# Kernel optimization log

Measured on AMD Instinct MI355X. Metric: run time of the kernel, lower is better.

The kernel has to match this reference:

```python
import jax, jax.numpy as jnp
import numpy as np

N = 100000   # nodes
E = 400000   # edges per relation
K = 2        # n_hop relations
D = 256      # in_dim
ATT = 64     # att_dim
L = 3        # n_layer
H1, H2 = 128, 64
EPS = 1e-5
NEG_SLOPE = 0.01


def setup_inputs() -> dict:
    key = jax.random.key(0)
    ks = jax.random.split(key, 16)
    s = 1.0 / np.sqrt(D)
    return {
        "x": jax.random.normal(ks[0], (N, D), jnp.float32),
        "edges_index": jax.random.randint(ks[1], (K, 2, E), 0, N),
        "edges_weight": jax.random.uniform(ks[2], (K, E), jnp.float32),
        "bn_gamma": jnp.ones((D,), jnp.float32),
        "bn_beta": jnp.zeros((D,), jnp.float32),
        "gcn_W": jax.random.normal(ks[3], (L, D, D), jnp.float32) * s,
        "gcn_b": jnp.zeros((L, D), jnp.float32),
        "att_lin_W": jax.random.normal(ks[4], (L, K, D, ATT), jnp.float32) * s,
        "att_lin_b": jnp.zeros((L, K, ATT), jnp.float32),
        "att_q": jax.random.normal(ks[5], (L, K, ATT), jnp.float32) * (1.0 / np.sqrt(ATT)),
        "proj_W1": jax.random.normal(ks[6], (D, H1), jnp.float32) * s,
        "proj_b1": jnp.zeros((H1,), jnp.float32),
        "proj_W2": jax.random.normal(ks[7], (H1, H2), jnp.float32) * (1.0 / np.sqrt(H1)),
        "proj_b2": jnp.zeros((H2,), jnp.float32),
    }


def _gcn_aggregate(row, col, w, xw):
    # symmetric gcn_norm on adj_t (add_self_loops=False):
    # deg[i] = sum of w over edges with col == i
    deg = jax.ops.segment_sum(w, col, num_segments=N)
    dinv = jnp.where(deg > 0, 1.0 / jnp.sqrt(deg), 0.0)
    norm = dinv[col] * w * dinv[row]                       # [E]
    # out[c] += norm * xw[r]
    return jax.ops.segment_sum(norm[:, None] * xw[row], col, num_segments=N)


def reference(x, edges_index, edges_weight, bn_gamma, bn_beta, gcn_W, gcn_b,
              att_lin_W, att_lin_b, att_q, proj_W1, proj_b1, proj_W2, proj_b2):
    # BatchNorm1d (training-mode batch stats)
    mu = jnp.mean(x, axis=0)
    var = jnp.mean((x - mu) ** 2, axis=0)
    h = (x - mu) / jnp.sqrt(var + EPS) * bn_gamma + bn_beta   # [N, D]

    rows = edges_index[:, 0, :]  # [K, E]
    cols = edges_index[:, 1, :]

    for i in range(L):
        xw = h @ gcn_W[i]                                     # shared transform [N, D]
        # per-relation sparse aggregation, vmapped over K
        xs = jax.vmap(_gcn_aggregate, in_axes=(0, 0, 0, None))(
            rows, cols, edges_weight, xw) + gcn_b[i]          # [K, N, D]
        # HanAtt: softmax over hops of per-node scores
        keys = jnp.tanh(jnp.einsum('knd,kdh->knh', xs, att_lin_W[i]) + att_lin_b[i][:, None, :])
        sim = jnp.einsum('knh,kh->kn', keys, att_q[i])        # [K, N]
        alpha = jax.nn.softmax(sim, axis=0)                   # softmax over K
        h = jnp.einsum('knd,kn->nd', xs, alpha)               # [N, D]
        h = jax.nn.relu(h)

    h = jax.nn.leaky_relu(h @ proj_W1 + proj_b1, NEG_SLOPE)
    h = jax.nn.leaky_relu(h @ proj_W2 + proj_b2, NEG_SLOPE)
    return h
```

## Files before the change

### kernel.cpp

```cpp
#include <hip/hip_runtime.h>
#include <hip/hip_bf16.h>
#include <math.h>

#define NN 100000
#define EE 400000
#define KD 2
#define DD 256
#define ATTD 64
#define LL 3
#define HH1 128
#define HH2 64
#define EPSV 1e-5f
#define SLOPE 0.01f
#define KN (KD * NN)
#define WFP 33554432.0f

typedef short short8 __attribute__((ext_vector_type(8)));
typedef float floatx4 __attribute__((ext_vector_type(4)));
typedef unsigned int u32x4 __attribute__((ext_vector_type(4)));
typedef unsigned short u16;
typedef unsigned int u32;
typedef unsigned long long u64;

__device__ __forceinline__ u16 f2bf(float f) {
    u32 u = __float_as_uint(f);
    return (u16)((u + 0x7fffu + ((u >> 16) & 1u)) >> 16);
}
__device__ __forceinline__ float bf2f(u16 h) {
    return __uint_as_float((u32)h << 16);
}

__device__ __forceinline__ void fma_row8_(float4& a0, float4& a1, uint4 w, float nv) {
    float2 f0 = __bfloat1622float2(*(const __hip_bfloat162*)&w.x);
    float2 f1 = __bfloat1622float2(*(const __hip_bfloat162*)&w.y);
    float2 f2 = __bfloat1622float2(*(const __hip_bfloat162*)&w.z);
    float2 f3 = __bfloat1622float2(*(const __hip_bfloat162*)&w.w);
    a0.x += nv * f0.x; a0.y += nv * f0.y; a0.z += nv * f1.x; a0.w += nv * f1.y;
    a1.x += nv * f2.x; a1.y += nv * f2.y; a1.z += nv * f3.x; a1.w += nv * f3.y;
}

__global__ void bn_stats(const float* __restrict__ x, float* __restrict__ sums) {
    int d = threadIdx.x;
    int r0 = blockIdx.x * 125;
    float s = 0.f, sq = 0.f;
    for (int r = r0; r < r0 + 125; ++r) {
        float v = x[(size_t)r * DD + d];
        s += v; sq += v * v;
    }
    atomicAdd(&sums[d], s);
    atomicAdd(&sums[DD + d], sq);
}

__global__ void bn_apply(const float* __restrict__ x, const float* __restrict__ sums,
                         const float* __restrict__ gamma, const float* __restrict__ beta,
                         u16* __restrict__ h_hi, u16* __restrict__ h_lo) {
    size_t i = (size_t)blockIdx.x * blockDim.x + threadIdx.x;
    const float inv_n = 1.f / NN;
    int dq = (int)(i & 63) * 4;
    float4 xv = ((const float4*)x)[i];
    ushort4 hv, lv;
    float* xp = (float*)&xv;
    u16* hp = (u16*)&hv; u16* lp = (u16*)&lv;
#pragma unroll
    for (int j = 0; j < 4; ++j) {
        int d = dq + j;
        float mu = sums[d] * inv_n;
        float var = sums[DD + d] * inv_n - mu * mu;
        float inv = rsqrtf(var + EPSV);
        float v = (xp[j] - mu) * inv * gamma[d] + beta[d];
        u16 hb = f2bf(v);
        hp[j] = hb;
        lp[j] = f2bf(v - bf2f(hb));
    }
    ((ushort4*)h_hi)[i] = hv;
    ((ushort4*)h_lo)[i] = lv;
}

__global__ void deg_count(const int* __restrict__ ei, const float* __restrict__ w,
                          u64* __restrict__ dc) {
    int i = blockIdx.x * blockDim.x + threadIdx.x;
    if (i >= KD * EE) return;
    int k = i / EE, e = i - k * EE;
    int col = ei[(size_t)k * 2 * EE + EE + e];
    u64 wfp = (u64)__float2uint_rn(w[i] * WFP);
    atomicAdd(&dc[k * NN + col], ((u64)1 << 32) | wfp);
}

__global__ void dinv_pack(const u64* __restrict__ dc, float* __restrict__ dinv,
                          int* __restrict__ starts) {
    int i = blockIdx.x * blockDim.x + threadIdx.x;
    if (i >= KN) return;
    u64 p = dc[i];
    float deg = (float)(u32)p * (1.f / WFP);
    dinv[i] = deg > 0.f ? 1.f / sqrtf(deg) : 0.f;
    starts[i] = (int)(p >> 32);
}

#define SCAN_NB ((KN + 255) / 256)
__global__ void scan_blocks(int* __restrict__ starts, int* __restrict__ bsums) {
    __shared__ int tmp[256];
    int t = threadIdx.x;
    int idx = blockIdx.x * 256 + t;
    int v = (idx < KN) ? starts[idx] : 0;
    tmp[t] = v;
    __syncthreads();
#pragma unroll
    for (int off = 1; off < 256; off <<= 1) {
        int s = (t >= off) ? tmp[t - off] : 0;
        __syncthreads();
        tmp[t] += s;
        __syncthreads();
    }
    if (idx < KN) starts[idx] = tmp[t] - v;
    if (t == 255) bsums[blockIdx.x] = tmp[255];
}

__global__ void scan_sums(int* __restrict__ bsums) {
    __shared__ int tmp[1024];
    int t = threadIdx.x;
    int v = (t < SCAN_NB) ? bsums[t] : 0;
    tmp[t] = v;
    __syncthreads();
#pragma unroll
    for (int off = 1; off < 1024; off <<= 1) {
        int s = (t >= off) ? tmp[t - off] : 0;
        __syncthreads();
        tmp[t] += s;
        __syncthreads();
    }
    if (t < SCAN_NB) bsums[t] = tmp[t] - v;
}

__global__ void scan_add(int* __restrict__ starts, const int* __restrict__ bsums) {
    int idx = blockIdx.x * 256 + threadIdx.x;
    if (idx < KN) starts[idx] += bsums[blockIdx.x];
}

__global__ void csr_fill(const int* __restrict__ ei, const float* __restrict__ w,
                         const float* __restrict__ dinv,
                         int* __restrict__ starts, int2* __restrict__ edata) {
    int i = blockIdx.x * blockDim.x + threadIdx.x;
    if (i >= KD * EE) return;
    int k = i / EE, e = i - k * EE;
    const int* eik = ei + (size_t)k * 2 * EE;
    int row = eik[e], col = eik[EE + e];
    float nv = dinv[k * NN + col] * w[i] * dinv[k * NN + row];
    int pos = atomicAdd(&starts[k * NN + col], 1);
    edata[pos] = make_int2(row, __float_as_int(nv));
}

#define GCN_T (LL * DD * DD)
#define ATT_T (LL * KD * DD * ATTD)
#define P1_T  (DD * HH1)
#define P2_T  (HH1 * HH2)
#define WC_TOTAL (GCN_T + ATT_T + P1_T + P2_T)
__device__ __forceinline__ void wconv1(const float* __restrict__ W, u16* __restrict__ Wt,
                                       int i, int Kd, int Nc) {
    int kk = i / Nc, n = i - kk * Nc;
    Wt[(size_t)n * Kd + kk] = f2bf(W[i]);
}
__global__ void wconv_all(const float* __restrict__ gcnW, u16* __restrict__ gcnWb,
                          const float* __restrict__ attW, u16* __restrict__ attWb,
                          const float* __restrict__ pW1, u16* __restrict__ pW1b,
                          const float* __restrict__ pW2, u16* __restrict__ pW2b) {
    int gid = blockIdx.x * 256 + threadIdx.x;
    if (gid >= WC_TOTAL) return;
    if (gid < GCN_T) {
        int l = gid >> 16, i = gid & 65535;
        wconv1(gcnW + (size_t)l * DD * DD, gcnWb + (size_t)l * DD * DD, i, DD, DD);
    } else if (gid < GCN_T + ATT_T) {
        int g = gid - GCN_T;
        int lk = g >> 14, i = g & 16383;
        wconv1(attW + (size_t)lk * DD * ATTD, attWb + (size_t)lk * ATTD * DD, i, DD, ATTD);
    } else if (gid < GCN_T + ATT_T + P1_T) {
        wconv1(pW1, pW1b, gid - (GCN_T + ATT_T), DD, HH1);
    } else {
        wconv1(pW2, pW2b, gid - (GCN_T + ATT_T + P1_T), HH1, HH2);
    }
}

__global__ void att_bias_fold(const float* __restrict__ attW, const float* __restrict__ attb,
                              const float* __restrict__ gcnb, float* __restrict__ batt) {
    int lk = blockIdx.x;
    int a = threadIdx.x;
    int l = lk >> 1;
    const float* W = attW + (size_t)lk * DD * ATTD;
    const float* gb = gcnb + l * DD;
    float s = attb[lk * ATTD + a];
    for (int d = 0; d < DD; ++d) s += gb[d] * W[d * ATTD + a];
    batt[lk * ATTD + a] = s;
}

#define LDSP 40

template<int BN_, int MODE, bool PRESPLIT, bool BIAS, int ACT>
__global__ __launch_bounds__(256) void gemm_mfma(
        const float* __restrict__ A,
        const u16* __restrict__ Ahi, const u16* __restrict__ Alo,
        const u16* __restrict__ Bt, const float* __restrict__ bias,
        float* __restrict__ Cf, u16* __restrict__ Cb,
        int M, int Kd, int Nc) {
    constexpr int JW = BN_ / 64;
    __shared__ u16 AsHi[64 * LDSP];
    __shared__ u16 AsLo[64 * LDSP];
    __shared__ u16 Bs[BN_ * LDSP];

    const int tid = threadIdx.x;
    const int lane = tid & 63, wx = tid >> 6;
    const int lane15 = lane & 15, quad = lane >> 4;
    const int bm = blockIdx.x * 64;
    const int bn = blockIdx.y * BN_;

    floatx4 acc[4][JW];
#pragma unroll
    for (int i = 0; i < 4; ++i)
#pragma unroll
        for (int j = 0; j < JW; ++j) acc[i][j] = (floatx4){0.f, 0.f, 0.f, 0.f};

    for (int k0 = 0; k0 < Kd; k0 += 32) {
        if constexpr (PRESPLIT) {
            {
                int m = tid >> 2, ko = (tid & 3) << 3;
                uint4 vh = make_uint4(0, 0, 0, 0), vl = make_uint4(0, 0, 0, 0);
                if (bm + m < M) {
                    vh = *(const uint4*)(Ahi + (size_t)(bm + m) * Kd + k0 + ko);
                    vl = *(const uint4*)(Alo + (size_t)(bm + m) * Kd + k0 + ko);
                }
                *(uint4*)(void*)(AsHi + m * LDSP + ko) = vh;
                *(uint4*)(void*)(AsLo + m * LDSP + ko) = vl;
            }
        } else {
#pragma unroll
            for (int t = tid; t < 512; t += 256) {
                int m = t >> 3, k4 = (t & 7) << 2;
                float4 v = make_float4(0.f, 0.f, 0.f, 0.f);
                if (bm + m < M) v = *(const float4*)(A + (size_t)(bm + m) * Kd + k0 + k4);
                u16 h0 = f2bf(v.x), h1 = f2bf(v.y), h2 = f2bf(v.z), h3 = f2bf(v.w);
                *(ushort4*)(void*)(AsHi + m * LDSP + k4) = make_ushort4(h0, h1, h2, h3);
                u16 l0 = f2bf(v.x - bf2f(h0)), l1 = f2bf(v.y - bf2f(h1));
                u16 l2 = f2bf(v.z - bf2f(h2)), l3 = f2bf(v.w - bf2f(h3));
                *(ushort4*)(void*)(AsLo + m * LDSP + k4) = make_ushort4(l0, l1, l2, l3);
            }
        }
#pragma unroll
        for (int t = tid; t < BN_ * 4; t += 256) {
            int n = t >> 2, ko = (t & 3) << 3;
            uint4 w = *(const uint4*)(Bt + (size_t)(bn + n) * Kd + k0 + ko);
            *(uint4*)(void*)(Bs + n * LDSP + ko) = w;
        }
        __syncthreads();

        const u16* pA  = AsHi + lane15 * LDSP + quad * 8;
        const u16* pAl = AsLo + lane15 * LDSP + quad * 8;
        const u16* pB  = Bs + (wx * (BN_ / 4) + lane15) * LDSP + quad * 8;
        short8 b[JW];
#pragma unroll
        for (int j = 0; j < JW; ++j) b[j] = *(const short8*)(pB + j * 16 * LDSP);
#pragma unroll
        for (int i = 0; i < 4; ++i) {
            short8 a = *(const short8*)(pA + i * 16 * LDSP);
#pragma unroll
            for (int j = 0; j < JW; ++j)
                acc[i][j] = __builtin_amdgcn_mfma_f32_16x16x32_bf16(a, b[j], acc[i][j], 0, 0, 0);
        }
#pragma unroll
        for (int i = 0; i < 4; ++i) {
            short8 a = *(const short8*)(pAl + i * 16 * LDSP);
#pragma unroll
            for (int j = 0; j < JW; ++j)
                acc[i][j] = __builtin_amdgcn_mfma_f32_16x16x32_bf16(a, b[j], acc[i][j], 0, 0, 0);
        }
        __syncthreads();
    }

#pragma unroll
    for (int i = 0; i < 4; ++i) {
#pragma unroll
        for (int r = 0; r < 4; ++r) {
            int row = bm + i * 16 + quad * 4 + r;
            if (row >= M) continue;
#pragma unroll
            for (int j = 0; j < JW; ++j) {
                int col = bn + wx * (BN_ / 4) + j * 16 + lane15;
                float v = acc[i][j][r];
                if constexpr (BIAS) v += bias[col];
                if constexpr (ACT == 1) v = v > 0.f ? v : SLOPE * v;
                if constexpr (MODE == 0) Cf[(size_t)row * Nc + col] = v;
                else                     Cb[(size_t)row * Nc + col] = f2bf(v);
            }
        }
    }
}

#define BMF 32
#define ALDS 264

__global__ __launch_bounds__(256) void att_fused(
        const int* __restrict__ starts, const int2* __restrict__ edata,
        const u16* __restrict__ xw, const u16* __restrict__ Bt,
        const float* __restrict__ batt, const float* __restrict__ qv,
        const float* __restrict__ gcnb,
        u16* __restrict__ h_hi, u16* __restrict__ h_lo) {
    __shared__ u16 As[KD * BMF * ALDS];
    __shared__ u16 Bs[2 * 64 * LDSP];
    __shared__ float simbuf[KD][2][BMF];

    const int tid = threadIdx.x;
    const int lane = tid & 63, waveid = tid >> 6;
    const int l32 = tid & 31;
    const int hid = tid >> 5;
    const int base = lane & 32;
    const int bm = blockIdx.x * BMF;

    {
        const int kk = hid >> 2;
        const int r0 = (hid & 3) * 8;
        const int widx0 = kk * NN + bm + r0;
        int sv = 0;
        if (l32 < 9) {
            int idx = widx0 - 1 + l32;
            sv = idx >= 0 ? starts[idx] : 0;
        }
        int2 ed[8];
#pragma unroll
        for (int g = 0; g < 8; ++g) {
            int b = __shfl(sv, base + g), e = __shfl(sv, base + g + 1);
            ed[g] = (l32 < e - b) ? edata[b + l32] : make_int2(0, 0);
        }
#pragma unroll
        for (int g = 0; g < 8; ++g) {
            int b = __shfl(sv, base + g), e = __shfl(sv, base + g + 1);
            int deg = e - b;
            int dmain = deg > 32 ? 32 : deg;
            float4 a0 = make_float4(0.f, 0.f, 0.f, 0.f);
            float4 a1 = make_float4(0.f, 0.f, 0.f, 0.f);
            int j = 0;
            for (; j + 4 <= dmain; j += 4) {
                int s0 = __shfl(ed[g].x, base + j),     s1 = __shfl(ed[g].x, base + j + 1);
                int s2 = __shfl(ed[g].x, base + j + 2), s3 = __shfl(ed[g].x, base + j + 3);
                float n0 = __int_as_float(__shfl(ed[g].y, base + j));
                float n1 = __int_as_float(__shfl(ed[g].y, base + j + 1));
                float n2 = __int_as_float(__shfl(ed[g].y, base + j + 2));
                float n3 = __int_as_float(__shfl(ed[g].y, base + j + 3));
                uint4 w0 = *(const uint4*)(xw + (size_t)s0 * DD + l32 * 8);
                uint4 w1 = *(const uint4*)(xw + (size_t)s1 * DD + l32 * 8);
                uint4 w2 = *(const uint4*)(xw + (size_t)s2 * DD + l32 * 8);
                uint4 w3 = *(const uint4*)(xw + (size_t)s3 * DD + l32 * 8);
                fma_row8_(a0, a1, w0, n0);
                fma_row8_(a0, a1, w1, n1);
                fma_row8_(a0, a1, w2, n2);
                fma_row8_(a0, a1, w3, n3);
            }
            for (; j < dmain; ++j) {
                int s0 = __shfl(ed[g].x, base + j);
                float nv = __int_as_float(__shfl(ed[g].y, base + j));
                uint4 w = *(const uint4*)(xw + (size_t)s0 * DD + l32 * 8);
                fma_row8_(a0, a1, w, nv);
            }
            for (int e2 = b + 32; e2 < e; ++e2) {
                int2 ee = edata[e2];
                float nv = __int_as_float(ee.y);
                uint4 w = *(const uint4*)(xw + (size_t)ee.x * DD + l32 * 8);
                fma_row8_(a0, a1, w, nv);
            }
            u32x4 st;
            st.x = (u32)f2bf(a0.x) | ((u32)f2bf(a0.y) << 16);
            st.y = (u32)f2bf(a0.z) | ((u32)f2bf(a0.w) << 16);
            st.z = (u32)f2bf(a1.x) | ((u32)f2bf(a1.y) << 16);
            st.w = (u32)f2bf(a1.z) | ((u32)f2bf(a1.w) << 16);
            *(u32x4*)(void*)(As + (kk * BMF + r0 + g) * ALDS + l32 * 8) = st;
        }
    }
    __syncthreads();

    const int kw = waveid >> 1, ch = waveid & 1;
    const int lane15 = lane & 15, quad = lane >> 4;
    floatx4 acc[2][2];
#pragma unroll
    for (int i = 0; i < 2; ++i)
#pragma unroll
        for (int j = 0; j < 2; ++j) acc[i][j] = (floatx4){0.f, 0.f, 0.f, 0.f};

    for (int k0 = 0; k0 < DD; k0 += 32) {
#pragma unroll
        for (int it = 0; it < 2; ++it) {
            int t = tid + it * 256;
            int k = t >> 8, c = (t >> 2) & 63, ko = (t & 3) << 3;
            uint4 v = *(const uint4*)(Bt + ((size_t)k * ATTD + c) * DD + k0 + ko);
            *(uint4*)(void*)(Bs + (k * 64 + c) * LDSP + ko) = v;
        }
        __syncthreads();
        const u16* pA = As + (kw * BMF + lane15) * ALDS + k0 + quad * 8;
        const u16* pB = Bs + (kw * 64 + ch * 32 + lane15) * LDSP + quad * 8;
        short8 b0 = *(const short8*)(pB);
        short8 b1 = *(const short8*)(pB + 16 * LDSP);
#pragma unroll
        for (int i = 0; i < 2; ++i) {
            short8 a = *(const short8*)(pA + i * 16 * ALDS);
            acc[i][0] = __builtin_amdgcn_mfma_f32_16x16x32_bf16(a, b0, acc[i][0], 0, 0, 0);
            acc[i][1] = __builtin_amdgcn_mfma_f32_16x16x32_bf16(a, b1, acc[i][1], 0, 0, 0);
        }
        __syncthreads();
    }

#pragma unroll
    for (int i = 0; i < 2; ++i) {
#pragma unroll
        for (int r = 0; r < 4; ++r) {
            float p = 0.f;
#pragma unroll
            for (int j = 0; j < 2; ++j) {
                int col = ch * 32 + j * 16 + lane15;
                float v = acc[i][j][r] + batt[kw * ATTD + col];
                float ex = __expf(2.f * v);
                float th = 1.f - 2.f / (ex + 1.f);
                p += th * qv[kw * ATTD + col];
            }
            p += __shfl_xor(p, 1, 64);
            p += __shfl_xor(p, 2, 64);
            p += __shfl_xor(p, 4, 64);
            p += __shfl_xor(p, 8, 64);
            if (lane15 == 0) simbuf[kw][ch][i * 16 + quad * 4 + r] = p;
        }
    }
    __syncthreads();

#pragma unroll
    for (int it = 0; it < 4; ++it) {
        int item = tid + it * 256;
        int row = item >> 5, c8 = item & 31;
        int grow = bm + row;
        float s0 = simbuf[0][0][row] + simbuf[0][1][row];
        float s1 = simbuf[1][0][row] + simbuf[1][1][row];
        float m = fmaxf(s0, s1);
        float e0 = __expf(s0 - m), e1 = __expf(s1 - m);
        float inv = 1.f / (e0 + e1);
        float a0 = e0 * inv, a1 = e1 * inv;
        uint4 x0 = *(const uint4*)(As + row * ALDS + c8 * 8);
        uint4 x1 = *(const uint4*)(As + (BMF + row) * ALDS + c8 * 8);
        const float* bp = gcnb + c8 * 8;
        uint4 hiw, low;
        u16* hp = (u16*)&hiw; u16* lp = (u16*)&low;
        const u32* xp0 = (const u32*)&x0; const u32* xp1 = (const u32*)&x1;
#pragma unroll
        for (int j = 0; j < 4; ++j) {
            float2 f0 = __bfloat1622float2(*(const __hip_bfloat162*)&xp0[j]);
            float2 f1 = __bfloat1622float2(*(const __hip_bfloat162*)&xp1[j]);
            float ra = fmaxf(0.f, a0 * f0.x + a1 * f1.x + bp[2 * j]);
            float rb = fmaxf(0.f, a0 * f0.y + a1 * f1.y + bp[2 * j + 1]);
            u16 ha = f2bf(ra), hb = f2bf(rb);
            hp[2 * j] = ha; hp[2 * j + 1] = hb;
            lp[2 * j] = f2bf(ra - bf2f(ha));
            lp[2 * j + 1] = f2bf(rb - bf2f(hb));
        }
        *(uint4*)(h_hi + (size_t)grow * DD + c8 * 8) = hiw;
        *(uint4*)(h_lo + (size_t)grow * DD + c8 * 8) = low;
    }
}

extern "C" void kernel_launch(void* const* d_in, const int* in_sizes, int n_in,
                              void* d_out, int out_size, void* d_ws, size_t ws_size,
                              hipStream_t stream) {
    const float* x     = (const float*)d_in[0];
    const int*   ei    = (const int*)d_in[1];
    const float* ew    = (const float*)d_in[2];
    const float* gamma = (const float*)d_in[3];
    const float* beta  = (const float*)d_in[4];
    const float* gcn_W = (const float*)d_in[5];
    const float* gcn_b = (const float*)d_in[6];
    const float* att_W = (const float*)d_in[7];
    const float* att_b = (const float*)d_in[8];
    const float* att_q = (const float*)d_in[9];
    const float* pW1   = (const float*)d_in[10];
    const float* pb1   = (const float*)d_in[11];
    const float* pW2   = (const float*)d_in[12];
    const float* pb2   = (const float*)d_in[13];
    float* out = (float*)d_out;

    char* wsb = (char*)d_ws;
    size_t off = 0;
    auto alloc = [&](size_t bytes) -> void* {
        void* p = wsb + off;
        off += (bytes + 255) & ~(size_t)255;
        return p;
    };
    u16*   h_hi  = (u16*)alloc((size_t)NN * DD * 2);
    u16*   h_lo  = (u16*)alloc((size_t)NN * DD * 2);
    u16*   xw    = (u16*)alloc((size_t)NN * DD * 2);
    float* p1tmp = (float*)xw;
    float* dinv  = (float*)alloc((size_t)KN * 4);
    int*   starts= (int*)alloc(((size_t)KN + 1) * 4);
    u64*   dc    = (u64*)alloc((size_t)KN * 8);
    int2*  edata = (int2*)alloc((size_t)KD * EE * 8);
    float* bnsums= (float*)alloc(2 * DD * 4);
    u16*   gcnWb = (u16*)alloc((size_t)LL * DD * DD * 2);
    u16*   attWb = (u16*)alloc((size_t)LL * KD * ATTD * DD * 2);
    u16*   pW1b  = (u16*)alloc((size_t)HH1 * DD * 2);
    u16*   pW2b  = (u16*)alloc((size_t)HH2 * HH1 * 2);
    float* batt  = (float*)alloc((size_t)LL * KD * ATTD * 4);
    int*   bsums = (int*)alloc((size_t)SCAN_NB * 4);

    wconv_all<<<(WC_TOTAL + 255) / 256, 256, 0, stream>>>(
        gcn_W, gcnWb, att_W, attWb, pW1, pW1b, pW2, pW2b);
    att_bias_fold<<<LL * KD, ATTD, 0, stream>>>(att_W, att_b, gcn_b, batt);

    hipMemsetAsync(bnsums, 0, 2 * DD * 4, stream);
    bn_stats<<<800, 256, 0, stream>>>(x, bnsums);
    bn_apply<<<25000, 256, 0, stream>>>(x, bnsums, gamma, beta, h_hi, h_lo);

    hipMemsetAsync(dc, 0, (size_t)KN * 8, stream);
    deg_count<<<(KD * EE + 255) / 256, 256, 0, stream>>>(ei, ew, dc);
    dinv_pack<<<(KN + 255) / 256, 256, 0, stream>>>(dc, dinv, starts);
    scan_blocks<<<SCAN_NB, 256, 0, stream>>>(starts, bsums);
    scan_sums<<<1, 1024, 0, stream>>>(bsums);
    scan_add<<<SCAN_NB, 256, 0, stream>>>(starts, bsums);
    csr_fill<<<(KD * EE + 255) / 256, 256, 0, stream>>>(ei, ew, dinv, starts, edata);

    const int MB64 = (NN + 63) / 64;
    const int MBF  = NN / BMF;
    for (int l = 0; l < LL; ++l) {
        gemm_mfma<256, 1, true, false, 0><<<dim3(MB64, 1), 256, 0, stream>>>(
            nullptr, h_hi, h_lo, gcnWb + (size_t)l * DD * DD, nullptr,
            nullptr, xw, NN, DD, DD);
        att_fused<<<MBF, 256, 0, stream>>>(
            starts, edata, xw, attWb + (size_t)l * KD * ATTD * DD,
            batt + (size_t)l * KD * ATTD, att_q + (size_t)l * KD * ATTD,
            gcn_b + l * DD, h_hi, h_lo);
    }

    gemm_mfma<128, 0, true, true, 1><<<dim3(MB64, 1), 256, 0, stream>>>(
        nullptr, h_hi, h_lo, pW1b, pb1, p1tmp, nullptr, NN, DD, HH1);
    gemm_mfma<64, 0, false, true, 1><<<dim3(MB64, 1), 256, 0, stream>>>(
        p1tmp, nullptr, nullptr, pW2b, pb2, out, nullptr, NN, HH1, HH2);
}
```

Measured before the change: 911.8 us.

## Interleave two nodes' gathers and read attention weights directly from global

The SpMM gather loop now handles two destination rows at once, so eight independent xw row loads are in flight per iteration instead of four, which raises memory-level parallelism. The attention GEMM no longer stages Bt through shared memory with per-step barriers. Each wave loads its B fragments straight from global/L2 into registers, which removes the LDS buffer and sixteen syncthreads. The trade-off is higher register pressure from the dual accumulators and uncoalesced, repeated global reads of the small weight matrix.

```diff
diff --git a/kernel.cpp b/kernel.cpp
--- a/kernel.cpp
+++ b/kernel.cpp
@@ -302,7 +302,6 @@
         const float* __restrict__ gcnb,
         u16* __restrict__ h_hi, u16* __restrict__ h_lo) {
     __shared__ u16 As[KD * BMF * ALDS];
-    __shared__ u16 Bs[2 * 64 * LDSP];
     __shared__ float simbuf[KD][2][BMF];
 
     const int tid = threadIdx.x;
@@ -328,47 +327,113 @@
             ed[g] = (l32 < e - b) ? edata[b + l32] : make_int2(0, 0);
         }
 #pragma unroll
-        for (int g = 0; g < 8; ++g) {
-            int b = __shfl(sv, base + g), e = __shfl(sv, base + g + 1);
-            int deg = e - b;
-            int dmain = deg > 32 ? 32 : deg;
-            float4 a0 = make_float4(0.f, 0.f, 0.f, 0.f);
-            float4 a1 = make_float4(0.f, 0.f, 0.f, 0.f);
+        for (int g = 0; g < 8; g += 2) {
+            int bA = __shfl(sv, base + g),     eA = __shfl(sv, base + g + 1);
+            int eB = __shfl(sv, base + g + 2);
+            int bB = eA;
+            int dA = eA - bA, dB = eB - bB;
+            int mA = dA > 32 ? 32 : dA, mB = dB > 32 ? 32 : dB;
+            float4 xa0 = make_float4(0.f,0.f,0.f,0.f), xa1 = make_float4(0.f,0.f,0.f,0.f);
+            float4 xb0 = make_float4(0.f,0.f,0.f,0.f), xb1 = make_float4(0.f,0.f,0.f,0.f);
             int j = 0;
-            for (; j + 4 <= dmain; j += 4) {
-                int s0 = __shfl(ed[g].x, base + j),     s1 = __shfl(ed[g].x, base + j + 1);
-                int s2 = __shfl(ed[g].x, base + j + 2), s3 = __shfl(ed[g].x, base + j + 3);
-                float n0 = __int_as_float(__shfl(ed[g].y, base + j));
-                float n1 = __int_as_float(__shfl(ed[g].y, base + j + 1));
-                float n2 = __int_as_float(__shfl(ed[g].y, base + j + 2));
-                float n3 = __int_as_float(__shfl(ed[g].y, base + j + 3));
-                uint4 w0 = *(const uint4*)(xw + (size_t)s0 * DD + l32 * 8);
-                uint4 w1 = *(const uint4*)(xw + (size_t)s1 * DD + l32 * 8);
-                uint4 w2 = *(const uint4*)(xw + (size_t)s2 * DD + l32 * 8);
-                uint4 w3 = *(const uint4*)(xw + (size_t)s3 * DD + l32 * 8);
-                fma_row8_(a0, a1, w0, n0);
-                fma_row8_(a0, a1, w1, n1);
-                fma_row8_(a0, a1, w2, n2);
-                fma_row8_(a0, a1, w3, n3);
-            }
-            for (; j < dmain; ++j) {
-                int s0 = __shfl(ed[g].x, base + j);
+            for (; j + 4 <= mA && j + 4 <= mB; j += 4) {
+                int ra0 = __shfl(ed[g].x, base + j),     ra1 = __shfl(ed[g].x, base + j + 1);
+                int ra2 = __shfl(ed[g].x, base + j + 2), ra3 = __shfl(ed[g].x, base + j + 3);
+                int rb0 = __shfl(ed[g+1].x, base + j),     rb1 = __shfl(ed[g+1].x, base + j + 1);
+                int rb2 = __shfl(ed[g+1].x, base + j + 2), rb3 = __shfl(ed[g+1].x, base + j + 3);
+                float na0 = __int_as_float(__shfl(ed[g].y, base + j));
+                float na1 = __int_as_float(__shfl(ed[g].y, base + j + 1));
+                float na2 = __int_as_float(__shfl(ed[g].y, base + j + 2));
+                float na3 = __int_as_float(__shfl(ed[g].y, base + j + 3));
+                float nb0 = __int_as_float(__shfl(ed[g+1].y, base + j));
+                float nb1 = __int_as_float(__shfl(ed[g+1].y, base + j + 1));
+                float nb2 = __int_as_float(__shfl(ed[g+1].y, base + j + 2));
+                float nb3 = __int_as_float(__shfl(ed[g+1].y, base + j + 3));
+                uint4 wa0 = *(const uint4*)(xw + (size_t)ra0 * DD + l32 * 8);
+                uint4 wa1 = *(const uint4*)(xw + (size_t)ra1 * DD + l32 * 8);
+                uint4 wa2 = *(const uint4*)(xw + (size_t)ra2 * DD + l32 * 8);
+                uint4 wa3 = *(const uint4*)(xw + (size_t)ra3 * DD + l32 * 8);
+                uint4 wb0 = *(const uint4*)(xw + (size_t)rb0 * DD + l32 * 8);
+                uint4 wb1 = *(const uint4*)(xw + (size_t)rb1 * DD + l32 * 8);
+                uint4 wb2 = *(const uint4*)(xw + (size_t)rb2 * DD + l32 * 8);
+                uint4 wb3 = *(const uint4*)(xw + (size_t)rb3 * DD + l32 * 8);
+                fma_row8_(xa0, xa1, wa0, na0);
+                fma_row8_(xa0, xa1, wa1, na1);
+                fma_row8_(xa0, xa1, wa2, na2);
+                fma_row8_(xa0, xa1, wa3, na3);
+                fma_row8_(xb0, xb1, wb0, nb0);
+                fma_row8_(xb0, xb1, wb1, nb1);
+                fma_row8_(xb0, xb1, wb2, nb2);
+                fma_row8_(xb0, xb1, wb3, nb3);
+            }
+            int jb = j;
+            for (; j + 4 <= mA; j += 4) {
+                int ra0 = __shfl(ed[g].x, base + j),     ra1 = __shfl(ed[g].x, base + j + 1);
+                int ra2 = __shfl(ed[g].x, base + j + 2), ra3 = __shfl(ed[g].x, base + j + 3);
+                float na0 = __int_as_float(__shfl(ed[g].y, base + j));
+                float na1 = __int_as_float(__shfl(ed[g].y, base + j + 1));
+                float na2 = __int_as_float(__shfl(ed[g].y, base + j + 2));
+                float na3 = __int_as_float(__shfl(ed[g].y, base + j + 3));
+                uint4 wa0 = *(const uint4*)(xw + (size_t)ra0 * DD + l32 * 8);
+                uint4 wa1 = *(const uint4*)(xw + (size_t)ra1 * DD + l32 * 8);
+                uint4 wa2 = *(const uint4*)(xw + (size_t)ra2 * DD + l32 * 8);
+                uint4 wa3 = *(const uint4*)(xw + (size_t)ra3 * DD + l32 * 8);
+                fma_row8_(xa0, xa1, wa0, na0);
+                fma_row8_(xa0, xa1, wa1, na1);
+                fma_row8_(xa0, xa1, wa2, na2);
+                fma_row8_(xa0, xa1, wa3, na3);
+            }
+            for (; j < mA; ++j) {
+                int r = __shfl(ed[g].x, base + j);
                 float nv = __int_as_float(__shfl(ed[g].y, base + j));
-                uint4 w = *(const uint4*)(xw + (size_t)s0 * DD + l32 * 8);
-                fma_row8_(a0, a1, w, nv);
-            }
-            for (int e2 = b + 32; e2 < e; ++e2) {
+                uint4 w = *(const uint4*)(xw + (size_t)r * DD + l32 * 8);
+                fma_row8_(xa0, xa1, w, nv);
+            }
+            for (; jb + 4 <= mB; jb += 4) {
+                int rb0 = __shfl(ed[g+1].x, base + jb),     rb1 = __shfl(ed[g+1].x, base + jb + 1);
+                int rb2 = __shfl(ed[g+1].x, base + jb + 2), rb3 = __shfl(ed[g+1].x, base + jb + 3);
+                float nb0 = __int_as_float(__shfl(ed[g+1].y, base + jb));
+                float nb1 = __int_as_float(__shfl(ed[g+1].y, base + jb + 1));
+                float nb2 = __int_as_float(__shfl(ed[g+1].y, base + jb + 2));
+                float nb3 = __int_as_float(__shfl(ed[g+1].y, base + jb + 3));
+                uint4 wb0 = *(const uint4*)(xw + (size_t)rb0 * DD + l32 * 8);
+                uint4 wb1 = *(const uint4*)(xw + (size_t)rb1 * DD + l32 * 8);
+                uint4 wb2 = *(const uint4*)(xw + (size_t)rb2 * DD + l32 * 8);
+                uint4 wb3 = *(const uint4*)(xw + (size_t)rb3 * DD + l32 * 8);
+                fma_row8_(xb0, xb1, wb0, nb0);
+                fma_row8_(xb0, xb1, wb1, nb1);
+                fma_row8_(xb0, xb1, wb2, nb2);
+                fma_row8_(xb0, xb1, wb3, nb3);
+            }
+            for (; jb < mB; ++jb) {
+                int r = __shfl(ed[g+1].x, base + jb);
+                float nv = __int_as_float(__shfl(ed[g+1].y, base + jb));
+                uint4 w = *(const uint4*)(xw + (size_t)r * DD + l32 * 8);
+                fma_row8_(xb0, xb1, w, nv);
+            }
+            for (int e2 = bA + 32; e2 < eA; ++e2) {
                 int2 ee = edata[e2];
                 float nv = __int_as_float(ee.y);
                 uint4 w = *(const uint4*)(xw + (size_t)ee.x * DD + l32 * 8);
-                fma_row8_(a0, a1, w, nv);
+                fma_row8_(xa0, xa1, w, nv);
+            }
+            for (int e2 = bB + 32; e2 < eB; ++e2) {
+                int2 ee = edata[e2];
+                float nv = __int_as_float(ee.y);
+                uint4 w = *(const uint4*)(xw + (size_t)ee.x * DD + l32 * 8);
+                fma_row8_(xb0, xb1, w, nv);
             }
             u32x4 st;
-            st.x = (u32)f2bf(a0.x) | ((u32)f2bf(a0.y) << 16);
-            st.y = (u32)f2bf(a0.z) | ((u32)f2bf(a0.w) << 16);
-            st.z = (u32)f2bf(a1.x) | ((u32)f2bf(a1.y) << 16);
-            st.w = (u32)f2bf(a1.z) | ((u32)f2bf(a1.w) << 16);
+            st.x = (u32)f2bf(xa0.x) | ((u32)f2bf(xa0.y) << 16);
+            st.y = (u32)f2bf(xa0.z) | ((u32)f2bf(xa0.w) << 16);
+            st.z = (u32)f2bf(xa1.x) | ((u32)f2bf(xa1.y) << 16);
+            st.w = (u32)f2bf(xa1.z) | ((u32)f2bf(xa1.w) << 16);
             *(u32x4*)(void*)(As + (kk * BMF + r0 + g) * ALDS + l32 * 8) = st;
+            st.x = (u32)f2bf(xb0.x) | ((u32)f2bf(xb0.y) << 16);
+            st.y = (u32)f2bf(xb0.z) | ((u32)f2bf(xb0.w) << 16);
+            st.z = (u32)f2bf(xb1.x) | ((u32)f2bf(xb1.y) << 16);
+            st.w = (u32)f2bf(xb1.z) | ((u32)f2bf(xb1.w) << 16);
+            *(u32x4*)(void*)(As + (kk * BMF + r0 + g + 1) * ALDS + l32 * 8) = st;
         }
     }
     __syncthreads();
@@ -381,26 +446,19 @@
 #pragma unroll
         for (int j = 0; j < 2; ++j) acc[i][j] = (floatx4){0.f, 0.f, 0.f, 0.f};
 
+    const u16* pB0 = Bt + (size_t)kw * ATTD * DD + (size_t)(ch * 32 + lane15) * DD + quad * 8;
+    const u16* pB1 = pB0 + 16 * DD;
+#pragma unroll
     for (int k0 = 0; k0 < DD; k0 += 32) {
-#pragma unroll
-        for (int it = 0; it < 2; ++it) {
-            int t = tid + it * 256;
-            int k = t >> 8, c = (t >> 2) & 63, ko = (t & 3) << 3;
-            uint4 v = *(const uint4*)(Bt + ((size_t)k * ATTD + c) * DD + k0 + ko);
-            *(uint4*)(void*)(Bs + (k * 64 + c) * LDSP + ko) = v;
-        }
-        __syncthreads();
+        short8 b0 = *(const short8*)(pB0 + k0);
+        short8 b1 = *(const short8*)(pB1 + k0);
         const u16* pA = As + (kw * BMF + lane15) * ALDS + k0 + quad * 8;
-        const u16* pB = Bs + (kw * 64 + ch * 32 + lane15) * LDSP + quad * 8;
-        short8 b0 = *(const short8*)(pB);
-        short8 b1 = *(const short8*)(pB + 16 * LDSP);
 #pragma unroll
         for (int i = 0; i < 2; ++i) {
             short8 a = *(const short8*)(pA + i * 16 * ALDS);
             acc[i][0] = __builtin_amdgcn_mfma_f32_16x16x32_bf16(a, b0, acc[i][0], 0, 0, 0);
             acc[i][1] = __builtin_amdgcn_mfma_f32_16x16x32_bf16(a, b1, acc[i][1], 0, 0, 0);
         }
-        __syncthreads();
     }
 
 #pragma unroll
```

Result: no change. 904.7 us (-0.8%).
